# Optimization experiments

Measured on AMD Instinct MI355X. Metric: run time of the kernel, lower is better.

The kernel has to match this reference:

```python
import jax, jax.numpy as jnp
import numpy as np

# Faithful GCN forward (eval mode, dropout = identity).
# GraphConvolution(x, adj): adj @ (x @ W) + b
# GraphConvolution_edge(edge_feat, adj): edge_feat = cat(x_i, x_j) over all (i,j) pairs,
#   support = edge_feat @ W  (shape [N*N, H]), out[i] = sum_j adj[i,j] * support[i,j] + b.
# materialized: out = (x @ W_top) * rowsum(adj)[:, None] + adj @ (x @ W_bot) + b.

N, NFEAT, NHID = 1536, 512, 64

def _edge_conv(x, adj, W, b):
    H = x.shape[-1]
    A = x @ W[:H]          # [N, H] contribution of x_i
    B = x @ W[H:]          # [N, H] contribution of x_j
    deg = jnp.sum(adj, axis=1, keepdims=True)  # [N, 1]
    return A * deg + adj @ B + b


def setup_inputs() -> dict:
    key = jax.random.key(0)
    ks = jax.random.split(key, 10)
    s1 = 1.0 / np.sqrt(NFEAT)
    s2 = 1.0 / np.sqrt(2 * NHID)
    return {
        "x_init": jax.random.normal(ks[0], (N, NFEAT), jnp.float32),
        "adj": jax.random.uniform(ks[1], (N, N), jnp.float32) / N,
        "adj1": jax.random.uniform(ks[2], (N, N), jnp.float32) / N,
        "fully_connected_graph": jnp.ones((N, N), jnp.float32),
        "W1": jax.random.uniform(ks[3], (NFEAT, NHID), jnp.float32, -s1, s1),
        "b1": jax.random.uniform(ks[4], (NHID,), jnp.float32, -s1, s1),
        "W2": jax.random.uniform(ks[5], (2 * NHID, NHID), jnp.float32, -s2, s2),
        "b2": jax.random.uniform(ks[6], (NHID,), jnp.float32, -s2, s2),
        "W3": jax.random.uniform(ks[7], (2 * NHID, NHID), jnp.float32, -s2, s2),
        "b3": jax.random.uniform(ks[8], (NHID,), jnp.float32, -s2, s2),
    }


def reference(x_init, adj, adj1, fully_connected_graph, W1, b1, W2, b2, W3, b3):
    # gc1: node graph conv + relu (dropout is identity in eval)
    x = jax.nn.relu(adj1 @ (x_init @ W1) + b1)          # [N, NHID]
    # gc_e2: pairwise edge conv + elu
    x = jax.nn.elu(_edge_conv(x, adj1, W2, b2))          # [N, NHID]
    # gc_e3: pairwise edge conv (no activation)
    x = _edge_conv(x, adj1, W3, b3)                      # [N, NHID]
    return jax.nn.log_softmax(x, axis=1)
```

## Files before the change

### kernel.cpp

```cpp
#include <hip/hip_runtime.h>
#include <cmath>

constexpr int NN   = 1536;
constexpr int FF   = 512;
constexpr int HH   = 64;
constexpr int RPB  = 16;
constexpr int NB   = NN / RPB;
constexpr int NT   = 1024;
constexpr int KST  = NN / 32;
constexpr int KST1 = FF / 32;

using f32x4  = __attribute__((ext_vector_type(4))) float;
using bf16x8 = __attribute__((ext_vector_type(8))) short;
using u16x4  = __attribute__((ext_vector_type(4))) unsigned short;
typedef unsigned short u16;

__device__ __forceinline__ u16 f2bf(float f) {
  unsigned u = __builtin_bit_cast(unsigned, f);
  return (u16)((u + 0x7fffu + ((u >> 16) & 1u)) >> 16);
}

__device__ __forceinline__ size_t bidx(int k, int c) {
  return (size_t)((c >> 5) * (KST * 2) + (k >> 5) * 2 + ((c >> 4) & 1)) * 512 +
         ((k & 31) >> 3) * 128 + (c & 15) * 8 + (k & 7);
}

__device__ __forceinline__ void gl_lds16(const void* g, void* l) {
  __builtin_amdgcn_global_load_lds(
      (const __attribute__((address_space(1))) unsigned*)g,
      (__attribute__((address_space(3))) unsigned*)l, 16, 0, 0);
}

__device__ __forceinline__ void pack_wnb(u16* WnB, const float* Wsrc, int tid) {
  int jp = tid & 127, kb = (tid >> 7) * 8;
  int srow0 = (jp >> 6) * 64, col = jp & 63;
#pragma unroll
  for (int i = 0; i < 8; ++i) {
    int k = kb + i;
    WnB[((k >> 5) * 8 + (jp >> 4)) * 512 + ((k & 31) >> 3) * 128 +
        (jp & 15) * 8 + (k & 7)] = f2bf(Wsrc[(size_t)(srow0 + k) * HH + col]);
  }
}

__global__ __launch_bounds__(NT, 4) void k_pre(
    const float* __restrict__ x, const float* __restrict__ adj,
    const float* __restrict__ W1,
    u16* __restrict__ adjT, u16* __restrict__ t1T, float* __restrict__ deg) {
  __shared__ u16 Al[KST1 * 512];
  __shared__ u16 Bl[KST1 * 4 * 512];
  __shared__ u16 Jl[KST * 512];
  __shared__ float red0[4][4][16][16];
  const int tid = threadIdx.x, lane = tid & 63, wave = tid >> 6;
  const int i0 = blockIdx.x * RPB;

  {
    int j0 = lane * 8;
    const float4* src = (const float4*)(x + (size_t)(i0 + wave) * FF + j0);
    float4 f0 = src[0], f1 = src[1];
    bf16x8 v;
    v[0] = (short)f2bf(f0.x); v[1] = (short)f2bf(f0.y);
    v[2] = (short)f2bf(f0.z); v[3] = (short)f2bf(f0.w);
    v[4] = (short)f2bf(f1.x); v[5] = (short)f2bf(f1.y);
    v[6] = (short)f2bf(f1.z); v[7] = (short)f2bf(f1.w);
    *(bf16x8*)&Al[(j0 >> 5) * 512 + ((j0 & 31) >> 3) * 128 + wave * 8] = v;
  }
  {
    int k = tid >> 1, c0 = (tid & 1) * 32;
    const float4* src = (const float4*)(W1 + (size_t)k * HH + c0);
    int base = (k >> 5) * 2048 + ((k & 31) >> 3) * 128 + (k & 7);
#pragma unroll
    for (int g = 0; g < 8; ++g) {
      float4 f = src[g];
      int c = c0 + g * 4;
      int off = base + (c >> 4) * 512 + (c & 15) * 8;
      Bl[off]      = f2bf(f.x);
      Bl[off + 8]  = f2bf(f.y);
      Bl[off + 16] = f2bf(f.z);
      Bl[off + 24] = f2bf(f.w);
    }
  }
  {
    int j0 = lane * 24;
    const float4* src = (const float4*)(adj + (size_t)(i0 + wave) * NN + j0);
    float4 f[6];
#pragma unroll
    for (int g = 0; g < 6; ++g) f[g] = src[g];
    float ds = 0.f;
#pragma unroll
    for (int g = 0; g < 6; ++g) ds += f[g].x + f[g].y + f[g].z + f[g].w;
#pragma unroll
    for (int g = 0; g < 3; ++g) {
      bf16x8 v;
      v[0] = (short)f2bf(f[g * 2].x);     v[1] = (short)f2bf(f[g * 2].y);
      v[2] = (short)f2bf(f[g * 2].z);     v[3] = (short)f2bf(f[g * 2].w);
      v[4] = (short)f2bf(f[g * 2 + 1].x); v[5] = (short)f2bf(f[g * 2 + 1].y);
      v[6] = (short)f2bf(f[g * 2 + 1].z); v[7] = (short)f2bf(f[g * 2 + 1].w);
      int k = j0 + g * 8;
      *(bf16x8*)&Jl[(k >> 5) * 512 + ((k & 31) >> 3) * 128 + wave * 8] = v;
    }
#pragma unroll
    for (int off = 32; off; off >>= 1) ds += __shfl_xor(ds, off, 64);
    if (lane == 0) deg[i0 + wave] = ds;
  }
  __syncthreads();

  {
    const float4* srcv = (const float4*)Jl;
    float4* dstv = (float4*)(adjT + (size_t)blockIdx.x * KST * 512);
#pragma unroll
    for (int s = 0; s < 3; ++s) dstv[tid + s * NT] = srcv[tid + s * NT];
  }
  {
    int ks = wave >> 2, cg = wave & 3;
    f32x4 acc = {0.f, 0.f, 0.f, 0.f};
#pragma unroll
    for (int s = 0; s < 4; ++s) {
      int t = ks * 4 + s;
      bf16x8 a = *(const bf16x8*)&Al[t * 512 + lane * 8];
      bf16x8 b = *(const bf16x8*)&Bl[(t * 4 + cg) * 512 + lane * 8];
      acc = __builtin_amdgcn_mfma_f32_16x16x32_bf16(a, b, acc, 0, 0, 0);
    }
#pragma unroll
    for (int q = 0; q < 4; ++q)
      red0[ks][cg][(lane >> 4) * 4 + q][lane & 15] = acc[q];
  }
  __syncthreads();
  {
    int r = wave, c = lane;
    float v = red0[0][c >> 4][r][c & 15] + red0[1][c >> 4][r][c & 15] +
              red0[2][c >> 4][r][c & 15] + red0[3][c >> 4][r][c & 15];
    t1T[bidx(i0 + r, c)] = f2bf(v);
  }
}

template <int MODE>
__global__ __launch_bounds__(NT, 4) void k_layer(
    const u16* __restrict__ adjT, const u16* __restrict__ TT,
    const float* __restrict__ Ain, const float* __restrict__ deg,
    const float* __restrict__ bias, const float* __restrict__ Wn,
    float* __restrict__ outA, u16* __restrict__ outBT,
    float* __restrict__ out) {
  __shared__ __attribute__((aligned(16))) char LB[155712];
  float* red8 = (float*)(LB + 98304);
  u16*   WnB  = (u16*)(LB + 133120);
  u16*   xA   = (u16*)(LB + 149504);
  float* xloc = (float*)(LB + 151552);

  const int tid = threadIdx.x, lane = tid & 63, wave = tid >> 6;
  const int i0 = blockIdx.x * RPB;

  const u16* ja = adjT + (size_t)blockIdx.x * (KST * 512);
  bf16x8 afr[3];
#pragma unroll
  for (int s = 0; s < 3; ++s)
    afr[s] = *(const bf16x8*)(ja + (wave * 3 + s) * 512 + lane * 8);

  if (MODE < 2) pack_wnb(WnB, Wn, tid);
  float dg = 0.f;
  if (MODE >= 1) dg = deg[i0 + wave];

  char* const regA = LB + wave * 6144;
  char* const regB = regA + 3072;
  const int kb = wave * 3;
  const char* tb = (const char*)TT + (size_t)lane * 16;

  f32x4 acc[4] = {};
#pragma unroll
  for (int s = 0; s < 3; ++s)
    gl_lds16(tb + (size_t)((kb + s) * 2 + 0) * 1024, regA + s * 1024);
#pragma unroll
  for (int s = 0; s < 3; ++s)
    gl_lds16(tb + (size_t)((kb + s) * 2 + 1) * 1024, regB + s * 1024);

#pragma unroll
  for (int cg = 0; cg < 4; ++cg) {
    if (cg < 3) asm volatile("s_waitcnt vmcnt(3)" ::: "memory");
    else        asm volatile("s_waitcnt vmcnt(0)" ::: "memory");
    __builtin_amdgcn_sched_barrier(0);
    char* reg = (cg & 1) ? regB : regA;
    bf16x8 b0 = *(const bf16x8*)(reg);
    bf16x8 b1 = *(const bf16x8*)(reg + 1024);
    bf16x8 b2 = *(const bf16x8*)(reg + 2048);
    asm volatile("s_waitcnt lgkmcnt(0)" ::: "memory");
    __builtin_amdgcn_sched_barrier(0);
    if (cg < 2) {
      int q = cg + 2;
#pragma unroll
      for (int s = 0; s < 3; ++s)
        gl_lds16(tb + (size_t)((q >> 1) * 96 + (kb + s) * 2 + (q & 1)) * 1024,
                 reg + s * 1024);
    }
    acc[cg] = __builtin_amdgcn_mfma_f32_16x16x32_bf16(afr[0], b0, acc[cg], 0, 0, 0);
    acc[cg] = __builtin_amdgcn_mfma_f32_16x16x32_bf16(afr[1], b1, acc[cg], 0, 0, 0);
    acc[cg] = __builtin_amdgcn_mfma_f32_16x16x32_bf16(afr[2], b2, acc[cg], 0, 0, 0);
  }

  if (wave < 8) {
#pragma unroll
    for (int cg = 0; cg < 4; ++cg)
#pragma unroll
      for (int q = 0; q < 4; ++q)
        red8[((wave * 4 + cg) * 16 + ((lane >> 4) * 4 + q)) * 17 +
             (lane & 15)] = acc[cg][q];
  }
  __syncthreads();
  if (wave >= 8) {
#pragma unroll
    for (int cg = 0; cg < 4; ++cg)
#pragma unroll
      for (int q = 0; q < 4; ++q)
        red8[(((wave - 8) * 4 + cg) * 16 + ((lane >> 4) * 4 + q)) * 17 +
             (lane & 15)] += acc[cg][q];
  }
  __syncthreads();

  {
    float v = bias[lane];
#pragma unroll
    for (int s = 0; s < 8; ++s)
      v += red8[((s * 4 + (lane >> 4)) * 16 + wave) * 17 + (lane & 15)];
    if (MODE >= 1) v += Ain[(size_t)(i0 + wave) * HH + lane] * dg;
    if (MODE == 0) v = fmaxf(v, 0.f);
    if (MODE == 1) v = v > 0.f ? v : expm1f(v);
    xloc[wave * 65 + lane] = v;
    if (MODE < 2)
      xA[(lane >> 5) * 512 + ((lane & 31) >> 3) * 128 + wave * 8 +
         (lane & 7)] = f2bf(v);
  }
  __syncthreads();

  if (MODE < 2) {
    if (wave < 8) {
      f32x4 a2 = {};
#pragma unroll
      for (int s = 0; s < 2; ++s) {
        bf16x8 a = *(const bf16x8*)&xA[s * 512 + lane * 8];
        bf16x8 b = *(const bf16x8*)&WnB[(s * 8 + wave) * 512 + lane * 8];
        a2 = __builtin_amdgcn_mfma_f32_16x16x32_bf16(a, b, a2, 0, 0, 0);
      }
      int row = (lane >> 4) * 4, colg = lane & 15;
      if (wave < 4) {
        int c = wave * 16 + colg;
#pragma unroll
        for (int q = 0; q < 4; ++q)
          outA[(size_t)(i0 + row + q) * HH + c] = a2[q];
      } else {
        int c = (wave - 4) * 16 + colg;
        u16x4 v;
#pragma unroll
        for (int q = 0; q < 4; ++q) v[q] = f2bf(a2[q]);
        *(u16x4*)&outBT[bidx(i0 + row, c)] = v;
      }
    }
  } else {
    float v = xloc[wave * 65 + lane];
    float m = v;
#pragma unroll
    for (int off = 32; off; off >>= 1) m = fmaxf(m, __shfl_xor(m, off, 64));
    float e = expf(v - m);
    float ssum = e;
#pragma unroll
    for (int off = 32; off; off >>= 1) ssum += __shfl_xor(ssum, off, 64);
    out[(size_t)(i0 + wave) * HH + lane] = v - m - logf(ssum);
  }
}

extern "C" void kernel_launch(void* const* d_in, const int* in_sizes, int n_in,
                              void* d_out, int out_size, void* d_ws,
                              size_t ws_size, hipStream_t stream) {
  const float* x   = (const float*)d_in[0];
  const float* adj = (const float*)d_in[2];
  const float* W1  = (const float*)d_in[4];
  const float* b1  = (const float*)d_in[5];
  const float* W2  = (const float*)d_in[6];
  const float* b2  = (const float*)d_in[7];
  const float* W3  = (const float*)d_in[8];
  const float* b3  = (const float*)d_in[9];
  float* out = (float*)d_out;

  char* ws = (char*)d_ws;
  u16* adjT = (u16*)ws;
  u16* t1T  = (u16*)(ws + 4718592);
  u16* B2T  = (u16*)(ws + 4915200);
  u16* B3T  = (u16*)(ws + 5111808);
  float* A2 = (float*)(ws + 5308416);
  float* A3 = (float*)(ws + 5701632);
  float* dg = (float*)(ws + 6094848);

  k_pre<<<NB, NT, 0, stream>>>(x, adj, W1, adjT, t1T, dg);
  k_layer<0><<<NB, NT, 0, stream>>>(adjT, t1T, nullptr, nullptr, b1, W2, A2,
                                    B2T, nullptr);
  k_layer<1><<<NB, NT, 0, stream>>>(adjT, B2T, A2, dg, b2, W3, A3, B3T,
                                    nullptr);
  k_layer<2><<<NB, NT, 0, stream>>>(adjT, B3T, A3, dg, b3, nullptr, nullptr,
                                    nullptr, out);
}
```

Baseline: 30.09 us.

## Read fp32 adjacency directly in each layer instead of a bf16 pre-pass copy

The pre-pass kernel no longer converts adj to a bf16 tiled copy and no longer computes degrees. Each layer kernel now loads its 16 rows of fp32 adj straight into MFMA A fragments, converting to bf16 in registers. Layers 1 and 2 also recompute row degrees through shuffles and LDS atomics. This removes the adjT write and the pre-pass dependency on adj, but each layer reads fp32 adj (twice the bytes of bf16) three times.

```diff
diff --git a/kernel.cpp b/kernel.cpp
--- a/kernel.cpp
+++ b/kernel.cpp
@@ -8,7 +8,6 @@
 constexpr int NB   = NN / RPB;
 constexpr int NT   = 1024;
 constexpr int KST  = NN / 32;
-constexpr int KST1 = FF / 32;
 
 using f32x4  = __attribute__((ext_vector_type(4))) float;
 using bf16x8 = __attribute__((ext_vector_type(8))) short;
@@ -42,14 +41,12 @@
   }
 }
 
-__global__ __launch_bounds__(NT, 4) void k_pre(
-    const float* __restrict__ x, const float* __restrict__ adj,
-    const float* __restrict__ W1,
-    u16* __restrict__ adjT, u16* __restrict__ t1T, float* __restrict__ deg) {
-  __shared__ u16 Al[KST1 * 512];
-  __shared__ u16 Bl[KST1 * 4 * 512];
-  __shared__ u16 Jl[KST * 512];
-  __shared__ float red0[4][4][16][16];
+__global__ __launch_bounds__(NT, 4) void k_t1(const float* __restrict__ x,
+                                              const float* __restrict__ W1,
+                                              u16* __restrict__ t1T) {
+  __shared__ u16 Al[16 * 512];
+  __shared__ u16 Bl[16 * 4 * 512];
+  __shared__ float red0[4][4][16][17];
   const int tid = threadIdx.x, lane = tid & 63, wave = tid >> 6;
   const int i0 = blockIdx.x * RPB;
 
@@ -79,37 +76,7 @@
       Bl[off + 24] = f2bf(f.w);
     }
   }
-  {
-    int j0 = lane * 24;
-    const float4* src = (const float4*)(adj + (size_t)(i0 + wave) * NN + j0);
-    float4 f[6];
-#pragma unroll
-    for (int g = 0; g < 6; ++g) f[g] = src[g];
-    float ds = 0.f;
-#pragma unroll
-    for (int g = 0; g < 6; ++g) ds += f[g].x + f[g].y + f[g].z + f[g].w;
-#pragma unroll
-    for (int g = 0; g < 3; ++g) {
-      bf16x8 v;
-      v[0] = (short)f2bf(f[g * 2].x);     v[1] = (short)f2bf(f[g * 2].y);
-      v[2] = (short)f2bf(f[g * 2].z);     v[3] = (short)f2bf(f[g * 2].w);
-      v[4] = (short)f2bf(f[g * 2 + 1].x); v[5] = (short)f2bf(f[g * 2 + 1].y);
-      v[6] = (short)f2bf(f[g * 2 + 1].z); v[7] = (short)f2bf(f[g * 2 + 1].w);
-      int k = j0 + g * 8;
-      *(bf16x8*)&Jl[(k >> 5) * 512 + ((k & 31) >> 3) * 128 + wave * 8] = v;
-    }
-#pragma unroll
-    for (int off = 32; off; off >>= 1) ds += __shfl_xor(ds, off, 64);
-    if (lane == 0) deg[i0 + wave] = ds;
-  }
-  __syncthreads();
-
-  {
-    const float4* srcv = (const float4*)Jl;
-    float4* dstv = (float4*)(adjT + (size_t)blockIdx.x * KST * 512);
-#pragma unroll
-    for (int s = 0; s < 3; ++s) dstv[tid + s * NT] = srcv[tid + s * NT];
-  }
+  __syncthreads();
   {
     int ks = wave >> 2, cg = wave & 3;
     f32x4 acc = {0.f, 0.f, 0.f, 0.f};
@@ -135,29 +102,45 @@
 
 template <int MODE>
 __global__ __launch_bounds__(NT, 4) void k_layer(
-    const u16* __restrict__ adjT, const u16* __restrict__ TT,
-    const float* __restrict__ Ain, const float* __restrict__ deg,
-    const float* __restrict__ bias, const float* __restrict__ Wn,
-    float* __restrict__ outA, u16* __restrict__ outBT,
-    float* __restrict__ out) {
-  __shared__ __attribute__((aligned(16))) char LB[155712];
-  float* red8 = (float*)(LB + 98304);
+    const float* __restrict__ adj, const u16* __restrict__ TT,
+    const float* __restrict__ Ain, const float* __restrict__ bias,
+    const float* __restrict__ Wn, float* __restrict__ outA,
+    u16* __restrict__ outBT, float* __restrict__ out) {
+  __shared__ __attribute__((aligned(16))) char LB[155776];
+  float* red  = (float*)(LB + 98304);
   u16*   WnB  = (u16*)(LB + 133120);
   u16*   xA   = (u16*)(LB + 149504);
   float* xloc = (float*)(LB + 151552);
+  float* degs = (float*)(LB + 155712);
 
   const int tid = threadIdx.x, lane = tid & 63, wave = tid >> 6;
   const int i0 = blockIdx.x * RPB;
 
-  const u16* ja = adjT + (size_t)blockIdx.x * (KST * 512);
+  if (MODE >= 1 && tid < RPB) degs[tid] = 0.f;
+
   bf16x8 afr[3];
-#pragma unroll
-  for (int s = 0; s < 3; ++s)
-    afr[s] = *(const bf16x8*)(ja + (wave * 3 + s) * 512 + lane * 8);
-
+  float dpart = 0.f;
+#pragma unroll
+  for (int s = 0; s < 3; ++s) {
+    const float4* ap = (const float4*)(adj + (size_t)(i0 + (lane & 15)) * NN +
+                                       (wave * 3 + s) * 32 + (lane >> 4) * 8);
+    float4 f0 = ap[0], f1 = ap[1];
+    if (MODE >= 1)
+      dpart += f0.x + f0.y + f0.z + f0.w + f1.x + f1.y + f1.z + f1.w;
+    bf16x8 v;
+    v[0] = (short)f2bf(f0.x); v[1] = (short)f2bf(f0.y);
+    v[2] = (short)f2bf(f0.z); v[3] = (short)f2bf(f0.w);
+    v[4] = (short)f2bf(f1.x); v[5] = (short)f2bf(f1.y);
+    v[6] = (short)f2bf(f1.z); v[7] = (short)f2bf(f1.w);
+    afr[s] = v;
+  }
   if (MODE < 2) pack_wnb(WnB, Wn, tid);
-  float dg = 0.f;
-  if (MODE >= 1) dg = deg[i0 + wave];
+  if (MODE >= 1) {
+    dpart += __shfl_xor(dpart, 16, 64);
+    dpart += __shfl_xor(dpart, 32, 64);
+    __syncthreads();
+    if (lane < 16) atomicAdd(&degs[lane], dpart);
+  }
 
   char* const regA = LB + wave * 6144;
   char* const regB = regA + 3072;
@@ -200,8 +183,8 @@
     for (int cg = 0; cg < 4; ++cg)
 #pragma unroll
       for (int q = 0; q < 4; ++q)
-        red8[((wave * 4 + cg) * 16 + ((lane >> 4) * 4 + q)) * 17 +
-             (lane & 15)] = acc[cg][q];
+        red[((wave * 4 + cg) * 16 + ((lane >> 4) * 4 + q)) * 17 +
+            (lane & 15)] = acc[cg][q];
   }
   __syncthreads();
   if (wave >= 8) {
@@ -209,8 +192,8 @@
     for (int cg = 0; cg < 4; ++cg)
 #pragma unroll
       for (int q = 0; q < 4; ++q)
-        red8[(((wave - 8) * 4 + cg) * 16 + ((lane >> 4) * 4 + q)) * 17 +
-             (lane & 15)] += acc[cg][q];
+        red[(((wave - 8) * 4 + cg) * 16 + ((lane >> 4) * 4 + q)) * 17 +
+            (lane & 15)] += acc[cg][q];
   }
   __syncthreads();
 
@@ -218,8 +201,8 @@
     float v = bias[lane];
 #pragma unroll
     for (int s = 0; s < 8; ++s)
-      v += red8[((s * 4 + (lane >> 4)) * 16 + wave) * 17 + (lane & 15)];
-    if (MODE >= 1) v += Ain[(size_t)(i0 + wave) * HH + lane] * dg;
+      v += red[((s * 4 + (lane >> 4)) * 16 + wave) * 17 + (lane & 15)];
+    if (MODE >= 1) v += Ain[(size_t)(i0 + wave) * HH + lane] * degs[wave];
     if (MODE == 0) v = fmaxf(v, 0.f);
     if (MODE == 1) v = v > 0.f ? v : expm1f(v);
     xloc[wave * 65 + lane] = v;
@@ -279,19 +262,16 @@
   float* out = (float*)d_out;
 
   char* ws = (char*)d_ws;
-  u16* adjT = (u16*)ws;
-  u16* t1T  = (u16*)(ws + 4718592);
-  u16* B2T  = (u16*)(ws + 4915200);
-  u16* B3T  = (u16*)(ws + 5111808);
-  float* A2 = (float*)(ws + 5308416);
-  float* A3 = (float*)(ws + 5701632);
-  float* dg = (float*)(ws + 6094848);
-
-  k_pre<<<NB, NT, 0, stream>>>(x, adj, W1, adjT, t1T, dg);
-  k_layer<0><<<NB, NT, 0, stream>>>(adjT, t1T, nullptr, nullptr, b1, W2, A2,
-                                    B2T, nullptr);
-  k_layer<1><<<NB, NT, 0, stream>>>(adjT, B2T, A2, dg, b2, W3, A3, B3T,
+  u16* t1T  = (u16*)ws;
+  u16* B2T  = (u16*)(ws + 196608);
+  u16* B3T  = (u16*)(ws + 393216);
+  float* A2 = (float*)(ws + 589824);
+  float* A3 = (float*)(ws + 983040);
+
+  k_t1<<<NB, NT, 0, stream>>>(x, W1, t1T);
+  k_layer<0><<<NB, NT, 0, stream>>>(adj, t1T, nullptr, b1, W2, A2, B2T,
                                     nullptr);
-  k_layer<2><<<NB, NT, 0, stream>>>(adjT, B3T, A3, dg, b3, nullptr, nullptr,
+  k_layer<1><<<NB, NT, 0, stream>>>(adj, B2T, A2, b2, W3, A3, B3T, nullptr);
+  k_layer<2><<<NB, NT, 0, stream>>>(adj, B3T, A3, b3, nullptr, nullptr,
                                     nullptr, out);
 }
```

After: 33.96 us. 12.9% more time.
